# Optimization experiments

Hardware: AMD Instinct MI355X
Metric: run time of the kernel (lower is better)

Reference implementation:

```python
import jax, jax.numpy as jnp
import numpy as np

B, S, D = 16, 1024, 512
H = 2048
E = 16
TOP_K = 4


def setup_inputs() -> dict:
    key = jax.random.key(0)
    ks = jax.random.split(key, 8)
    scale = 0.02
    x = jax.random.normal(ks[0], (B, S, D), dtype=jnp.float32)
    router_w = jax.random.normal(ks[1], (D, E), dtype=jnp.float32) * scale
    router_b = jax.random.normal(ks[2], (E,), dtype=jnp.float32) * scale
    w1 = jax.random.normal(ks[3], (E, D, H), dtype=jnp.float32) * scale
    b1 = jax.random.normal(ks[4], (E, H), dtype=jnp.float32) * scale
    w2 = jax.random.normal(ks[5], (E, H, D), dtype=jnp.float32) * scale
    b2 = jax.random.normal(ks[6], (E, D), dtype=jnp.float32) * scale
    return {"x": x, "router_w": router_w, "router_b": router_b,
            "w1": w1, "b1": b1, "w2": w2, "b2": b2}


def reference(x, router_w, router_b, w1, b1, w2, b2):
    # x: [B, S, D] -> flatten tokens
    x_flat = x.reshape(-1, D)                       # [T, D]
    logits = x_flat @ router_w + router_b           # [T, E]
    top_vals, top_idx = jax.lax.top_k(logits, TOP_K)  # [T, K]
    gates = jax.nn.softmax(top_vals, axis=-1)       # softmax over selected experts only
    # Combined per-expert gate weight per token: sum over k slots routed to e.
    onehot = jax.nn.one_hot(top_idx, E, dtype=x.dtype)  # [T, K, E]
    comb = jnp.einsum('tk,tke->te', gates, onehot)      # [T, E]
    out = jnp.zeros_like(x_flat)
    for e in range(E):  # fixed small expert count
        h = jax.nn.relu(x_flat @ w1[e] + b1[e])     # [T, H]
        y = h @ w2[e] + b2[e]                       # [T, D]
        out = out + comb[:, e:e + 1] * y
    return out.reshape(x.shape)
```

## Files before the change

kernel.cpp:

```cpp
#include <hip/hip_runtime.h>
#include <stdint.h>

#define T_TOK 16384
#define DIM 512
#define HID 2048
#define NE 16
#define TOPK 4
#define BM 256
#define BN 256
#define BKT 64
#define PAIR_CAP 69632
#define MAX_TILES 272
#define NB_CNT 64

typedef short s8v __attribute__((ext_vector_type(8)));
typedef float f4v __attribute__((ext_vector_type(4)));
typedef unsigned int u4v __attribute__((ext_vector_type(4)));

__device__ __forceinline__ unsigned short f2bf(float f) {
  unsigned int u = __builtin_bit_cast(unsigned int, f);
  u = (u + 0x7fffu + ((u >> 16) & 1u)) >> 16;
  return (unsigned short)u;
}
__device__ __forceinline__ float bf2f(unsigned short h) {
  return __builtin_bit_cast(float, (unsigned int)h << 16);
}

__device__ __forceinline__ void gload16(const void* g, void* l) {
  __builtin_amdgcn_global_load_lds(
      (const __attribute__((address_space(1))) unsigned int*)(uintptr_t)g,
      (__attribute__((address_space(3))) unsigned int*)(uintptr_t)l,
      16, 0, 0);
}

__global__ __launch_bounds__(256) void k_transpose_cast(const float* __restrict__ src,
                                                        unsigned short* __restrict__ dst,
                                                        int R, int C) {
  __shared__ float tile[32][33];
  size_t zo = (size_t)blockIdx.z * R * C;
  src += zo; dst += zo;
  int c0 = blockIdx.x * 32, r0 = blockIdx.y * 32;
  int tx = threadIdx.x, ty = threadIdx.y;
#pragma unroll
  for (int i = 0; i < 4; ++i)
    tile[ty + 8 * i][tx] = src[(size_t)(r0 + ty + 8 * i) * C + c0 + tx];
  __syncthreads();
#pragma unroll
  for (int i = 0; i < 4; ++i)
    dst[(size_t)(c0 + ty + 8 * i) * R + r0 + tx] = f2bf(tile[tx][ty + 8 * i]);
}

__global__ __launch_bounds__(256) void k_router(const float* __restrict__ x,
                                                const float* __restrict__ rw,
                                                const float* __restrict__ rb,
                                                int* __restrict__ topki,
                                                float* __restrict__ topkg,
                                                unsigned short* __restrict__ xb) {
  int wv = threadIdx.x >> 6, lane = threadIdx.x & 63;
  int t = blockIdx.x * 4 + wv;
  const float* xr = x + (size_t)t * DIM;
  unsigned short* xbr = xb + (size_t)t * DIM;
  double acc[NE];
#pragma unroll
  for (int e = 0; e < NE; ++e) acc[e] = 0.0;
  for (int it = 0; it < DIM / 64; ++it) {
    float xv = xr[it * 64 + lane];
    xbr[it * 64 + lane] = f2bf(xv);
    const float* r = rw + (size_t)(it * 64 + lane) * NE;
#pragma unroll
    for (int e = 0; e < NE; ++e) acc[e] += (double)xv * (double)r[e];
  }
#pragma unroll
  for (int off = 32; off >= 1; off >>= 1) {
#pragma unroll
    for (int e = 0; e < NE; ++e) acc[e] += __shfl_xor(acc[e], off, 64);
  }
  if (lane == 0) {
    float v[NE];
#pragma unroll
    for (int e = 0; e < NE; ++e) v[e] = (float)acc[e] + rb[e];
    int idx[TOPK]; float val[TOPK];
#pragma unroll
    for (int k = 0; k < TOPK; ++k) {
      float best = -1e30f; int bi = 0;
#pragma unroll
      for (int e = 0; e < NE; ++e)
        if (v[e] > best) { best = v[e]; bi = e; }
      idx[k] = bi; val[k] = best; v[bi] = -1e30f;
    }
    float m = val[0], s = 0.f, g[TOPK];
#pragma unroll
    for (int k = 0; k < TOPK; ++k) { g[k] = __expf(val[k] - m); s += g[k]; }
    float inv = 1.f / s;
#pragma unroll
    for (int k = 0; k < TOPK; ++k) {
      topki[t * TOPK + k] = idx[k];
      topkg[t * TOPK + k] = g[k] * inv;
    }
  }
}

__global__ __launch_bounds__(256) void k_count(const int* __restrict__ topki,
                                               int* __restrict__ meta) {
  __shared__ int lcnt[NE];
  int tid = threadIdx.x;
  if (tid < NE) lcnt[tid] = 0;
  __syncthreads();
  int base = blockIdx.x * 1024 + tid * 4;
#pragma unroll
  for (int j = 0; j < 4; ++j) atomicAdd(&lcnt[topki[base + j]], 1);
  __syncthreads();
  if (tid < NE) meta[1056 + blockIdx.x * NE + tid] = lcnt[tid];
}

__global__ __launch_bounds__(256) void k_plan(int* __restrict__ meta,
                                              int* __restrict__ ptok,
                                              float* __restrict__ pgate) {
  __shared__ int cnt_s[NE], po_s[NE + 1];
  int tid = threadIdx.x;
  if (tid < NE) {
    int s = 0;
    for (int b = 0; b < NB_CNT; ++b) s += meta[1056 + b * NE + tid];
    cnt_s[tid] = s;
  }
  __syncthreads();
  if (tid == 0) {
    int off = 0;
    for (int e = 0; e < NE; ++e) {
      po_s[e] = off;
      meta[1 + e] = off;
      off += ((cnt_s[e] + BM - 1) / BM) * BM;
    }
    po_s[NE] = off;
    meta[1 + NE] = off;
    meta[0] = off / BM;
  }
  __syncthreads();
  if (tid < NE) {
    int run = po_s[tid];
    for (int b = 0; b < NB_CNT; ++b) {
      meta[32 + b * NE + tid] = run;
      run += meta[1056 + b * NE + tid];
    }
  }
  for (int e = 0; e < NE; ++e) {
    int start = po_s[e] + cnt_s[e], end = po_s[e + 1];
    for (int i = start + tid; i < end; i += 256) { ptok[i] = 0; pgate[i] = 0.f; }
  }
}

__global__ __launch_bounds__(256) void k_scatter(const int* __restrict__ topki,
                                                 const float* __restrict__ topkg,
                                                 const int* __restrict__ meta,
                                                 int* __restrict__ ptok,
                                                 float* __restrict__ pgate,
                                                 int* __restrict__ sinv) {
  __shared__ int lcnt[NE];
  int tid = threadIdx.x;
  if (tid < NE) lcnt[tid] = 0;
  __syncthreads();
  int base = blockIdx.x * 1024 + tid * 4;
#pragma unroll
  for (int j = 0; j < 4; ++j) {
    int i = base + j;
    int e = topki[i];
    int r = atomicAdd(&lcnt[e], 1);
    int slot = meta[32 + blockIdx.x * NE + e] + r;
    ptok[slot] = i >> 2;
    pgate[slot] = topkg[i];
    sinv[i] = slot;
  }
}


#define MBAR() asm volatile("s_barrier" ::: "memory")
#define EBAR() asm volatile("s_barrier" ::: "memory")
#define SP1() __builtin_amdgcn_s_setprio(1)
#define SP0() __builtin_amdgcn_s_setprio(0)
#define LGK0() do { asm volatile("s_waitcnt lgkmcnt(0)" ::: "memory"); \
                    __builtin_amdgcn_sched_barrier(0); } while (0)
#define VMC(n) asm volatile("s_waitcnt vmcnt(" #n ")" ::: "memory")
#define NOP ((void)0)

#define STG(rg, kt, c) do {                                                            \
    int _k = (kt) * BKT;                                                               \
    if ((rg) < 2) {                                                                    \
      gload16(aP[rg][0] + _k, (char*)&Al[c][0] + (rg) * 16384 + w * 1024);             \
      gload16(aP[rg][1] + _k, (char*)&Al[c][0] + (rg) * 16384 + 8192 + w * 1024);      \
    } else {                                                                           \
      gload16(bP[(rg) - 2][0] + _k, (char*)&Bl[c][0] + ((rg) - 2) * 16384 + w * 1024); \
      gload16(bP[(rg) - 2][1] + _k, (char*)&Bl[c][0] + ((rg) - 2) * 16384 + 8192 + w * 1024); \
    }                                                                                  \
  } while (0)

#define RDA(c, mq) do {                                                                \
    _Pragma("unroll")                                                                  \
    for (int mt = 0; mt < 4; ++mt) {                                                   \
      af[mt][0] = __builtin_bit_cast(s8v, *(const u4v*)&Al[c][(mq) * 8192 + aoff + mt * 1024 + cs0]); \
      af[mt][1] = __builtin_bit_cast(s8v, *(const u4v*)&Al[c][(mq) * 8192 + aoff + mt * 1024 + cs1]); \
    }                                                                                  \
  } while (0)

#define RDB(c, nq) do {                                                                \
    _Pragma("unroll")                                                                  \
    for (int nt = 0; nt < 2; ++nt) {                                                   \
      bfr[nt][0] = __builtin_bit_cast(s8v, *(const u4v*)&Bl[c][(nq) * 8192 + boff + nt * 1024 + cs0]); \
      bfr[nt][1] = __builtin_bit_cast(s8v, *(const u4v*)&Bl[c][(nq) * 8192 + boff + nt * 1024 + cs1]); \
    }                                                                                  \
  } while (0)

#define MMQ(mq, nq) do {                                                               \
    _Pragma("unroll")                                                                  \
    for (int mt = 0; mt < 4; ++mt) {                                                   \
      _Pragma("unroll")                                                                \
      for (int nt = 0; nt < 2; ++nt) {                                                 \
        acc[(mq) * 4 + mt][(nq) * 2 + nt] = __builtin_amdgcn_mfma_f32_16x16x32_bf16(   \
            af[mt][0], bfr[nt][0], acc[(mq) * 4 + mt][(nq) * 2 + nt], 0, 0, 0);        \
        acc[(mq) * 4 + mt][(nq) * 2 + nt] = __builtin_amdgcn_mfma_f32_16x16x32_bf16(   \
            af[mt][1], bfr[nt][1], acc[(mq) * 4 + mt][(nq) * 2 + nt], 0, 0, 0);        \
      }                                                                                \
    }                                                                                  \
  } while (0)

#define PH(c, mq, nq, doA, STAGE, WAITC) do {  \
    if (doA) RDA(c, mq);                       \
    RDB(c, nq);                                \
    STAGE;                                     \
    MBAR();                                    \
    LGK0();                                    \
    SP1(); MMQ(mq, nq); SP0();                 \
    WAITC;                                     \
    EBAR();                                    \
  } while (0)

__global__ __launch_bounds__(512, 2) void k_pipe(const unsigned short* __restrict__ xb,
                                                 const unsigned short* __restrict__ w1t,
                                                 const float* __restrict__ b1,
                                                 const unsigned short* __restrict__ w2t,
                                                 const float* __restrict__ b2,
                                                 const int* __restrict__ ptok,
                                                 const float* __restrict__ pgate,
                                                 const int* __restrict__ meta,
                                                 unsigned short* __restrict__ hdst,
                                                 const unsigned short* __restrict__ hsrc,
                                                 unsigned short* __restrict__ yslot,
                                                 float* __restrict__ out,
                                                 int c1, int c2, int C) {
  __shared__ __align__(16) unsigned short Al[2][BM * BKT];
  __shared__ __align__(16) unsigned short Bl[2][BN * BKT];
  int tid = threadIdx.x;
  int lane = tid & 63, w = tid >> 6;
  int wm = w >> 2, wn = w & 3;
  int lrow = lane & 15, quad = lane >> 4;
  int r7 = lrow & 7;
  int sub = lane >> 3, lg = (lane & 7) ^ sub;

  bool g2 = blockIdx.x < 2;
  int chunk = g2 ? c2 : c1;
  if (chunk < 0) return;
  int tile = chunk * C + blockIdx.y;
  if (tile >= meta[0]) return;
  int row0 = tile * BM;
  int e = 0;
#pragma unroll
  for (int i = 1; i < NE; ++i)
    if (row0 >= meta[1 + i]) e = i;
  int nblock = g2 ? (int)blockIdx.x * BN : ((int)blockIdx.x - 2) * BN;

  const unsigned short* aP[2][2];
  const unsigned short* bP[2][2];
  int NKT;
  if (!g2) {
    NKT = DIM / BKT;
#pragma unroll
    for (int h = 0; h < 2; ++h)
#pragma unroll
      for (int t = 0; t < 2; ++t) {
        int r = h * 128 + t * 64 + w * 8 + sub;
        aP[h][t] = xb + (size_t)ptok[row0 + r] * DIM + lg * 8;
        bP[h][t] = w1t + ((size_t)e * HID + nblock + r) * DIM + lg * 8;
      }
  } else {
    NKT = HID / BKT;
#pragma unroll
    for (int h = 0; h < 2; ++h)
#pragma unroll
      for (int t = 0; t < 2; ++t) {
        int r = h * 128 + t * 64 + w * 8 + sub;
        aP[h][t] = hsrc + ((size_t)blockIdx.y * BM + r) * HID + lg * 8;
        bP[h][t] = w2t + ((size_t)e * DIM + nblock + r) * HID + lg * 8;
      }
  }

  int aoff = (wm * 64 + lrow) * BKT;
  int boff = (wn * 32 + lrow) * BKT;
  int cs0 = (quad ^ r7) * 8;
  int cs1 = ((4 + quad) ^ r7) * 8;

  f4v acc[8][4] = {};
  s8v af[4][2];
  s8v bfr[2][2];

  STG(0, 0, 0); STG(2, 0, 0); STG(1, 0, 0); STG(3, 0, 0);
  STG(0, 1, 1); STG(2, 1, 1);
  VMC(8);
  EBAR();

  int NI = NKT >> 1;
  for (int i = 0; i < NI - 1; ++i) {
    int bt = 2 * i;
    PH(0, 0, 0, true,  STG(1, bt + 1, 1), VMC(6));
    PH(0, 0, 1, false, STG(3, bt + 1, 1), NOP);
    PH(0, 1, 0, true,  STG(0, bt + 2, 0), NOP);
    PH(0, 1, 1, false, STG(2, bt + 2, 0), VMC(8));
    PH(1, 0, 0, true,  STG(1, bt + 2, 0), VMC(6));
    PH(1, 0, 1, false, STG(3, bt + 2, 0), NOP);
    PH(1, 1, 0, true,  STG(0, bt + 3, 1), NOP);
    PH(1, 1, 1, false, STG(2, bt + 3, 1), VMC(8));
  }
  {
    int bt = NKT - 2;
    PH(0, 0, 0, true,  STG(1, bt + 1, 1), VMC(6));
    PH(0, 0, 1, false, STG(3, bt + 1, 1), NOP);
    PH(0, 1, 0, true,  NOP, NOP);
    PH(0, 1, 1, false, NOP, VMC(4));
    PH(1, 0, 0, true,  NOP, VMC(0));
    PH(1, 0, 1, false, NOP, NOP);
    PH(1, 1, 0, true,  NOP, NOP);
    PH(1, 1, 1, false, NOP, NOP);
  }

  if (!g2) {
    size_t hrow0 = (size_t)blockIdx.y * BM;
#pragma unroll
    for (int nq = 0; nq < 2; ++nq) {
#pragma unroll
      for (int nt = 0; nt < 2; ++nt) {
        int gcol = nblock + nq * 128 + wn * 32 + nt * 16 + lrow;
        float bias = b1[e * HID + gcol];
#pragma unroll
        for (int mq = 0; mq < 2; ++mq) {
#pragma unroll
          for (int mt = 0; mt < 4; ++mt) {
#pragma unroll
            for (int j = 0; j < 4; ++j) {
              int grow = mq * 128 + wm * 64 + mt * 16 + quad * 4 + j;
              float v = acc[mq * 4 + mt][nq * 2 + nt][j] + bias;
              hdst[(hrow0 + grow) * HID + gcol] = f2bf(v > 0.f ? v : 0.f);
            }
          }
        }
      }
    }
  } else {
    float bias[2][2];
#pragma unroll
    for (int nq = 0; nq < 2; ++nq)
#pragma unroll
      for (int nt = 0; nt < 2; ++nt)
        bias[nq][nt] = b2[e * DIM + nblock + nq * 128 + wn * 32 + nt * 16 + lrow];
    if (yslot) {
#pragma unroll
      for (int mq = 0; mq < 2; ++mq) {
#pragma unroll
        for (int mt = 0; mt < 4; ++mt) {
#pragma unroll
          for (int j = 0; j < 4; ++j) {
            int p = row0 + mq * 128 + wm * 64 + mt * 16 + quad * 4 + j;
            float g = pgate[p];
            unsigned short* yr = yslot + (size_t)p * DIM + nblock + wn * 32 + lrow;
#pragma unroll
            for (int nq = 0; nq < 2; ++nq)
#pragma unroll
              for (int nt = 0; nt < 2; ++nt)
                yr[nq * 128 + nt * 16] = f2bf(g * (acc[mq * 4 + mt][nq * 2 + nt][j] + bias[nq][nt]));
          }
        }
      }
    } else {
#pragma unroll
      for (int mq = 0; mq < 2; ++mq) {
#pragma unroll
        for (int mt = 0; mt < 4; ++mt) {
#pragma unroll
          for (int j = 0; j < 4; ++j) {
            int p = row0 + mq * 128 + wm * 64 + mt * 16 + quad * 4 + j;
            float g = pgate[p];
            if (g != 0.f) {
              int tok = ptok[p];
              float* orow = out + (size_t)tok * DIM + nblock + wn * 32 + lrow;
#pragma unroll
              for (int nq = 0; nq < 2; ++nq)
#pragma unroll
                for (int nt = 0; nt < 2; ++nt)
                  atomicAdd(orow + nq * 128 + nt * 16, g * (acc[mq * 4 + mt][nq * 2 + nt][j] + bias[nq][nt]));
            }
          }
        }
      }
    }
  }
}

__global__ __launch_bounds__(256) void k_gather(const unsigned short* __restrict__ yslot,
                                                const int* __restrict__ sinv,
                                                float* __restrict__ out) {
  int id = blockIdx.x * 256 + threadIdx.x;
  int t = id >> 7, d4 = (id & 127) << 2;
  int4 s = *(const int4*)(sinv + t * 4);
  int sl[4] = {s.x, s.y, s.z, s.w};
  float sum0 = 0.f, sum1 = 0.f, sum2 = 0.f, sum3 = 0.f;
#pragma unroll
  for (int k = 0; k < 4; ++k) {
    ushort4 v = *(const ushort4*)(yslot + (size_t)sl[k] * DIM + d4);
    sum0 += bf2f(v.x); sum1 += bf2f(v.y); sum2 += bf2f(v.z); sum3 += bf2f(v.w);
  }
  float4 r; r.x = sum0; r.y = sum1; r.z = sum2; r.w = sum3;
  *(float4*)(out + (size_t)t * DIM + d4) = r;
}

extern "C" void kernel_launch(void* const* d_in, const int* in_sizes, int n_in,
                              void* d_out, int out_size, void* d_ws, size_t ws_size,
                              hipStream_t stream) {
  const float* x  = (const float*)d_in[0];
  const float* rw = (const float*)d_in[1];
  const float* rb = (const float*)d_in[2];
  const float* w1 = (const float*)d_in[3];
  const float* b1 = (const float*)d_in[4];
  const float* w2 = (const float*)d_in[5];
  const float* b2 = (const float*)d_in[6];
  float* out = (float*)d_out;
  char* ws = (char*)d_ws;

  size_t o_xb    = 0;
  size_t o_w1t   = o_xb    + (size_t)T_TOK * DIM * 2;
  size_t o_w2t   = o_w1t   + (size_t)NE * DIM * HID * 2;
  size_t o_topki = o_w2t   + (size_t)NE * DIM * HID * 2;
  size_t o_topkg = o_topki + (size_t)T_TOK * TOPK * 4;
  size_t o_meta  = o_topkg + (size_t)T_TOK * TOPK * 4;
  size_t o_ptok  = o_meta  + 16384;
  size_t o_pgate = o_ptok  + (size_t)PAIR_CAP * 4;
  size_t o_sinv  = o_pgate + (size_t)PAIR_CAP * 4;
  size_t o_yslot = o_sinv  + (size_t)T_TOK * TOPK * 4;
  size_t o_hb    = o_yslot + (size_t)PAIR_CAP * DIM * 2;

  unsigned short* xb   = (unsigned short*)(ws + o_xb);
  unsigned short* w1t  = (unsigned short*)(ws + o_w1t);
  unsigned short* w2t  = (unsigned short*)(ws + o_w2t);
  int*            tki  = (int*)(ws + o_topki);
  float*          tkg  = (float*)(ws + o_topkg);
  int*            meta = (int*)(ws + o_meta);
  int*            ptok = (int*)(ws + o_ptok);
  float*          pgt  = (float*)(ws + o_pgate);
  int*            sinv = (int*)(ws + o_sinv);

  size_t tile_h = (size_t)BM * HID * 2;
  size_t avail = ws_size > o_hb ? ws_size - o_hb : 0;
  long Cd = (long)(avail / (2 * tile_h));
  int use_slot = Cd >= 1;

  k_router<<<T_TOK / 4, 256, 0, stream>>>(x, rw, rb, tki, tkg, xb);
  k_transpose_cast<<<dim3(HID / 32, DIM / 32, NE), dim3(32, 8), 0, stream>>>(w1, w1t, DIM, HID);
  k_transpose_cast<<<dim3(DIM / 32, HID / 32, NE), dim3(32, 8), 0, stream>>>(w2, w2t, HID, DIM);
  k_count<<<NB_CNT, 256, 0, stream>>>(tki, meta);
  k_plan<<<1, 256, 0, stream>>>(meta, ptok, pgt);
  k_scatter<<<NB_CNT, 256, 0, stream>>>(tki, tkg, meta, ptok, pgt, sinv);

  if (use_slot) {
    unsigned short* ysl = (unsigned short*)(ws + o_yslot);
    int C = (int)(Cd > MAX_TILES ? MAX_TILES : Cd);
    int n_chunks = (MAX_TILES + C - 1) / C;
    unsigned short* hb0 = (unsigned short*)(ws + o_hb);
    unsigned short* hb1 = hb0 + (size_t)C * BM * HID;
    for (int i = 0; i <= n_chunks; ++i) {
      unsigned short* dst = (i & 1) ? hb1 : hb0;
      unsigned short* src = (i & 1) ? hb0 : hb1;
      int c1 = (i < n_chunks) ? i : -1;
      int c2 = i - 1;
      k_pipe<<<dim3(10, C), 512, 0, stream>>>(xb, w1t, b1, w2t, b2, ptok, pgt, meta,
                                              dst, src, ysl, out, c1, c2, C);
    }
    k_gather<<<T_TOK * DIM / 4 / 256, 256, 0, stream>>>(ysl, sinv, out);
  } else {
    long Cf = (long)((ws_size - o_yslot) / tile_h);
    int C = (int)(Cf < 1 ? 1 : (Cf > MAX_TILES ? MAX_TILES : Cf));
    int n_chunks = (MAX_TILES + C - 1) / C;
    unsigned short* hb = (unsigned short*)(ws + o_yslot);
    hipMemsetAsync(d_out, 0, (size_t)T_TOK * DIM * 4, stream);
    for (int i = 0; i < n_chunks; ++i) {
      k_pipe<<<dim3(10, C), 512, 0, stream>>>(xb, w1t, b1, w2t, b2, ptok, pgt, meta,
                                              hb, hb, nullptr, out, i, -1, C);
      k_pipe<<<dim3(10, C), 512, 0, stream>>>(xb, w1t, b1, w2t, b2, ptok, pgt, meta,
                                              hb, hb, nullptr, out, -1, i, C);
    }
  }
}
```

Baseline: 747.6 us.

## Use persistent blocks with an atomic work queue and a deeper LDS staging pipeline

Replaces the static 2D grid of GEMM tiles with 256 persistent blocks that pull work items from a global atomic counter. Second-GEMM items are ordered first, and per-launch counters are zeroed in the plan kernel. The K-loop is also restructured: B fragments are now held for both halves, and one more stage is issued before the loop, so loads overlap MFMA work more deeply. This aims to balance the uneven per-expert tile counts and cut tail idle time, at the cost of an atomic and a barrier per item plus extra register pressure.

Measured after the change: 676.3 us. 9.5% less time.

```diff
diff --git a/kernel.cpp b/kernel.cpp
--- a/kernel.cpp
+++ b/kernel.cpp
@@ -12,6 +12,7 @@
 #define PAIR_CAP 69632
 #define MAX_TILES 272
 #define NB_CNT 64
+#define QOFF 2080
 
 typedef short s8v __attribute__((ext_vector_type(8)));
 typedef float f4v __attribute__((ext_vector_type(4)));
@@ -118,6 +119,7 @@
                                               float* __restrict__ pgate) {
   __shared__ int cnt_s[NE], po_s[NE + 1];
   int tid = threadIdx.x;
+  for (int i = tid; i < 1024; i += 256) meta[QOFF + i] = 0;
   if (tid < NE) {
     int s = 0;
     for (int b = 0; b < NB_CNT; ++b) s += meta[1056 + b * NE + tid];
@@ -204,8 +206,8 @@
 #define RDB(c, nq) do {                                                                \
     _Pragma("unroll")                                                                  \
     for (int nt = 0; nt < 2; ++nt) {                                                   \
-      bfr[nt][0] = __builtin_bit_cast(s8v, *(const u4v*)&Bl[c][(nq) * 8192 + boff + nt * 1024 + cs0]); \
-      bfr[nt][1] = __builtin_bit_cast(s8v, *(const u4v*)&Bl[c][(nq) * 8192 + boff + nt * 1024 + cs1]); \
+      bfr[nq][nt][0] = __builtin_bit_cast(s8v, *(const u4v*)&Bl[c][(nq) * 8192 + boff + nt * 1024 + cs0]); \
+      bfr[nq][nt][1] = __builtin_bit_cast(s8v, *(const u4v*)&Bl[c][(nq) * 8192 + boff + nt * 1024 + cs1]); \
     }                                                                                  \
   } while (0)
 
@@ -215,39 +217,32 @@
       _Pragma("unroll")                                                                \
       for (int nt = 0; nt < 2; ++nt) {                                                 \
         acc[(mq) * 4 + mt][(nq) * 2 + nt] = __builtin_amdgcn_mfma_f32_16x16x32_bf16(   \
-            af[mt][0], bfr[nt][0], acc[(mq) * 4 + mt][(nq) * 2 + nt], 0, 0, 0);        \
+            af[mt][0], bfr[nq][nt][0], acc[(mq) * 4 + mt][(nq) * 2 + nt], 0, 0, 0);    \
         acc[(mq) * 4 + mt][(nq) * 2 + nt] = __builtin_amdgcn_mfma_f32_16x16x32_bf16(   \
-            af[mt][1], bfr[nt][1], acc[(mq) * 4 + mt][(nq) * 2 + nt], 0, 0, 0);        \
+            af[mt][1], bfr[nq][nt][1], acc[(mq) * 4 + mt][(nq) * 2 + nt], 0, 0, 0);    \
       }                                                                                \
     }                                                                                  \
   } while (0)
 
-#define PH(c, mq, nq, doA, STAGE, WAITC) do {  \
-    if (doA) RDA(c, mq);                       \
-    RDB(c, nq);                                \
-    STAGE;                                     \
-    MBAR();                                    \
-    LGK0();                                    \
-    SP1(); MMQ(mq, nq); SP0();                 \
-    WAITC;                                     \
-    EBAR();                                    \
-  } while (0)
-
-__global__ __launch_bounds__(512, 2) void k_pipe(const unsigned short* __restrict__ xb,
-                                                 const unsigned short* __restrict__ w1t,
-                                                 const float* __restrict__ b1,
-                                                 const unsigned short* __restrict__ w2t,
-                                                 const float* __restrict__ b2,
-                                                 const int* __restrict__ ptok,
-                                                 const float* __restrict__ pgate,
-                                                 const int* __restrict__ meta,
-                                                 unsigned short* __restrict__ hdst,
-                                                 const unsigned short* __restrict__ hsrc,
-                                                 unsigned short* __restrict__ yslot,
-                                                 float* __restrict__ out,
+#define TAIL(mq, nq) do { MBAR(); LGK0(); SP1(); MMQ(mq, nq); SP0(); } while (0)
+
+__global__ __launch_bounds__(512, 2) void k_pipe(const unsigned short* xb,
+                                                 const unsigned short* w1t,
+                                                 const float* b1,
+                                                 const unsigned short* w2t,
+                                                 const float* b2,
+                                                 const int* ptok,
+                                                 const float* pgate,
+                                                 const int* meta,
+                                                 int* qctr,
+                                                 unsigned short* hdst,
+                                                 const unsigned short* hsrc,
+                                                 unsigned short* yslot,
+                                                 float* out,
                                                  int c1, int c2, int C) {
   __shared__ __align__(16) unsigned short Al[2][BM * BKT];
   __shared__ __align__(16) unsigned short Bl[2][BN * BKT];
+  __shared__ int sh_item;
   int tid = threadIdx.x;
   int lane = tid & 63, w = tid >> 6;
   int wm = w >> 2, wn = w & 3;
@@ -255,145 +250,170 @@
   int r7 = lrow & 7;
   int sub = lane >> 3, lg = (lane & 7) ^ sub;
 
-  bool g2 = blockIdx.x < 2;
-  int chunk = g2 ? c2 : c1;
-  if (chunk < 0) return;
-  int tile = chunk * C + blockIdx.y;
-  if (tile >= meta[0]) return;
-  int row0 = tile * BM;
-  int e = 0;
-#pragma unroll
-  for (int i = 1; i < NE; ++i)
-    if (row0 >= meta[1 + i]) e = i;
-  int nblock = g2 ? (int)blockIdx.x * BN : ((int)blockIdx.x - 2) * BN;
-
-  const unsigned short* aP[2][2];
-  const unsigned short* bP[2][2];
-  int NKT;
-  if (!g2) {
-    NKT = DIM / BKT;
-#pragma unroll
-    for (int h = 0; h < 2; ++h)
-#pragma unroll
-      for (int t = 0; t < 2; ++t) {
-        int r = h * 128 + t * 64 + w * 8 + sub;
-        aP[h][t] = xb + (size_t)ptok[row0 + r] * DIM + lg * 8;
-        bP[h][t] = w1t + ((size_t)e * HID + nblock + r) * DIM + lg * 8;
-      }
-  } else {
-    NKT = HID / BKT;
-#pragma unroll
-    for (int h = 0; h < 2; ++h)
-#pragma unroll
-      for (int t = 0; t < 2; ++t) {
-        int r = h * 128 + t * 64 + w * 8 + sub;
-        aP[h][t] = hsrc + ((size_t)blockIdx.y * BM + r) * HID + lg * 8;
-        bP[h][t] = w2t + ((size_t)e * DIM + nblock + r) * HID + lg * 8;
-      }
-  }
-
   int aoff = (wm * 64 + lrow) * BKT;
   int boff = (wn * 32 + lrow) * BKT;
   int cs0 = (quad ^ r7) * 8;
   int cs1 = ((4 + quad) ^ r7) * 8;
 
-  f4v acc[8][4] = {};
-  s8v af[4][2];
-  s8v bfr[2][2];
-
-  STG(0, 0, 0); STG(2, 0, 0); STG(1, 0, 0); STG(3, 0, 0);
-  STG(0, 1, 1); STG(2, 1, 1);
-  VMC(8);
-  EBAR();
-
-  int NI = NKT >> 1;
-  for (int i = 0; i < NI - 1; ++i) {
-    int bt = 2 * i;
-    PH(0, 0, 0, true,  STG(1, bt + 1, 1), VMC(6));
-    PH(0, 0, 1, false, STG(3, bt + 1, 1), NOP);
-    PH(0, 1, 0, true,  STG(0, bt + 2, 0), NOP);
-    PH(0, 1, 1, false, STG(2, bt + 2, 0), VMC(8));
-    PH(1, 0, 0, true,  STG(1, bt + 2, 0), VMC(6));
-    PH(1, 0, 1, false, STG(3, bt + 2, 0), NOP);
-    PH(1, 1, 0, true,  STG(0, bt + 3, 1), NOP);
-    PH(1, 1, 1, false, STG(2, bt + 3, 1), VMC(8));
-  }
-  {
-    int bt = NKT - 2;
-    PH(0, 0, 0, true,  STG(1, bt + 1, 1), VMC(6));
-    PH(0, 0, 1, false, STG(3, bt + 1, 1), NOP);
-    PH(0, 1, 0, true,  NOP, NOP);
-    PH(0, 1, 1, false, NOP, VMC(4));
-    PH(1, 0, 0, true,  NOP, VMC(0));
-    PH(1, 0, 1, false, NOP, NOP);
-    PH(1, 1, 0, true,  NOP, NOP);
-    PH(1, 1, 1, false, NOP, NOP);
-  }
-
-  if (!g2) {
-    size_t hrow0 = (size_t)blockIdx.y * BM;
-#pragma unroll
-    for (int nq = 0; nq < 2; ++nq) {
-#pragma unroll
-      for (int nt = 0; nt < 2; ++nt) {
-        int gcol = nblock + nq * 128 + wn * 32 + nt * 16 + lrow;
-        float bias = b1[e * HID + gcol];
-#pragma unroll
-        for (int mq = 0; mq < 2; ++mq) {
-#pragma unroll
-          for (int mt = 0; mt < 4; ++mt) {
-#pragma unroll
-            for (int j = 0; j < 4; ++j) {
-              int grow = mq * 128 + wm * 64 + mt * 16 + quad * 4 + j;
-              float v = acc[mq * 4 + mt][nq * 2 + nt][j] + bias;
-              hdst[(hrow0 + grow) * HID + gcol] = f2bf(v > 0.f ? v : 0.f);
+  int T = meta[0];
+  int t2 = 0, t1 = 0;
+  if (c2 >= 0) { t2 = T - c2 * C; t2 = t2 < 0 ? 0 : (t2 > C ? C : t2); }
+  if (c1 >= 0) { t1 = T - c1 * C; t1 = t1 < 0 ? 0 : (t1 > C ? C : t1); }
+  int n2 = 2 * t2, nit = n2 + 8 * t1;
+
+  for (;;) {
+    if (tid == 0) sh_item = atomicAdd(qctr, 1);
+    __syncthreads();
+    int it = sh_item;
+    if (it >= nit) break;
+
+    bool g2 = it < n2;
+    int tloc, nb, tile;
+    if (g2) { tloc = it >> 1; nb = (it & 1) * BN; tile = c2 * C + tloc; }
+    else { int j = it - n2; tloc = j >> 3; nb = (j & 7) * BN; tile = c1 * C + tloc; }
+    int row0 = tile * BM;
+    int e = 0;
+#pragma unroll
+    for (int i2 = 1; i2 < NE; ++i2)
+      if (row0 >= meta[1 + i2]) e = i2;
+
+    const unsigned short* aP[2][2];
+    const unsigned short* bP[2][2];
+    int NKT;
+    if (!g2) {
+      NKT = DIM / BKT;
+#pragma unroll
+      for (int h = 0; h < 2; ++h)
+#pragma unroll
+        for (int t = 0; t < 2; ++t) {
+          int r = h * 128 + t * 64 + w * 8 + sub;
+          aP[h][t] = xb + (size_t)ptok[row0 + r] * DIM + lg * 8;
+          bP[h][t] = w1t + ((size_t)e * HID + nb + r) * DIM + lg * 8;
+        }
+    } else {
+      NKT = HID / BKT;
+#pragma unroll
+      for (int h = 0; h < 2; ++h)
+#pragma unroll
+        for (int t = 0; t < 2; ++t) {
+          int r = h * 128 + t * 64 + w * 8 + sub;
+          aP[h][t] = hsrc + ((size_t)tloc * BM + r) * HID + lg * 8;
+          bP[h][t] = w2t + ((size_t)e * DIM + nb + r) * HID + lg * 8;
+        }
+    }
+
+    f4v acc[8][4] = {};
+    s8v af[4][2];
+    s8v bfr[2][2][2];
+
+    STG(0, 0, 0); STG(2, 0, 0); STG(3, 0, 0); STG(1, 0, 0);
+    STG(0, 1, 1); STG(2, 1, 1); STG(3, 1, 1);
+    VMC(4);
+    EBAR();
+
+    int NI = NKT >> 1;
+    for (int i = 0; i < NI - 1; ++i) {
+      int bt = 2 * i;
+      RDA(0, 0); RDB(0, 0); STG(1, bt + 1, 1);
+      TAIL(0, 0); NOP; EBAR();
+      RDB(0, 1); STG(0, bt + 2, 0);
+      TAIL(0, 1); NOP; EBAR();
+      RDA(0, 1); STG(2, bt + 2, 0);
+      TAIL(1, 0); NOP; EBAR();
+      STG(3, bt + 2, 0);
+      TAIL(1, 1); VMC(6); EBAR();
+      RDA(1, 0); RDB(1, 0); STG(1, bt + 2, 0);
+      TAIL(0, 0); NOP; EBAR();
+      RDB(1, 1); STG(0, bt + 3, 1);
+      TAIL(0, 1); NOP; EBAR();
+      RDA(1, 1); STG(2, bt + 3, 1);
+      TAIL(1, 0); NOP; EBAR();
+      STG(3, bt + 3, 1);
+      TAIL(1, 1); VMC(6); EBAR();
+    }
+    {
+      int bt = NKT - 2;
+      RDA(0, 0); RDB(0, 0); STG(1, bt + 1, 1);
+      TAIL(0, 0); NOP; EBAR();
+      RDB(0, 1);
+      TAIL(0, 1); NOP; EBAR();
+      RDA(0, 1);
+      TAIL(1, 0); NOP; EBAR();
+      TAIL(1, 1); VMC(4); EBAR();
+      RDA(1, 0); RDB(1, 0);
+      TAIL(0, 0); VMC(2); EBAR();
+      RDB(1, 1);
+      TAIL(0, 1); VMC(0); EBAR();
+      RDA(1, 1);
+      TAIL(1, 0); NOP; EBAR();
+      TAIL(1, 1); NOP; EBAR();
+    }
+
+    if (!g2) {
+      size_t hrow0 = (size_t)tloc * BM;
+#pragma unroll
+      for (int nq = 0; nq < 2; ++nq) {
+#pragma unroll
+        for (int nt = 0; nt < 2; ++nt) {
+          int gcol = nb + nq * 128 + wn * 32 + nt * 16 + lrow;
+          float bias = b1[e * HID + gcol];
+#pragma unroll
+          for (int mq = 0; mq < 2; ++mq) {
+#pragma unroll
+            for (int mt = 0; mt < 4; ++mt) {
+#pragma unroll
+              for (int j = 0; j < 4; ++j) {
+                int grow = mq * 128 + wm * 64 + mt * 16 + quad * 4 + j;
+                float v = acc[mq * 4 + mt][nq * 2 + nt][j] + bias;
+                hdst[(hrow0 + grow) * HID + gcol] = f2bf(v > 0.f ? v : 0.f);
+              }
             }
           }
         }
       }
-    }
-  } else {
-    float bias[2][2];
-#pragma unroll
-    for (int nq = 0; nq < 2; ++nq)
-#pragma unroll
-      for (int nt = 0; nt < 2; ++nt)
-        bias[nq][nt] = b2[e * DIM + nblock + nq * 128 + wn * 32 + nt * 16 + lrow];
-    if (yslot) {
-#pragma unroll
-      for (int mq = 0; mq < 2; ++mq) {
-#pragma unroll
-        for (int mt = 0; mt < 4; ++mt) {
-#pragma unroll
-          for (int j = 0; j < 4; ++j) {
-            int p = row0 + mq * 128 + wm * 64 + mt * 16 + quad * 4 + j;
-            float g = pgate[p];
-            unsigned short* yr = yslot + (size_t)p * DIM + nblock + wn * 32 + lrow;
-#pragma unroll
-            for (int nq = 0; nq < 2; ++nq)
-#pragma unroll
-              for (int nt = 0; nt < 2; ++nt)
-                yr[nq * 128 + nt * 16] = f2bf(g * (acc[mq * 4 + mt][nq * 2 + nt][j] + bias[nq][nt]));
+    } else {
+      float bias[2][2];
+#pragma unroll
+      for (int nq = 0; nq < 2; ++nq)
+#pragma unroll
+        for (int nt = 0; nt < 2; ++nt)
+          bias[nq][nt] = b2[e * DIM + nb + nq * 128 + wn * 32 + nt * 16 + lrow];
+      if (yslot) {
+#pragma unroll
+        for (int mq = 0; mq < 2; ++mq) {
+#pragma unroll
+          for (int mt = 0; mt < 4; ++mt) {
+#pragma unroll
+            for (int j = 0; j < 4; ++j) {
+              int p = row0 + mq * 128 + wm * 64 + mt * 16 + quad * 4 + j;
+              float g = pgate[p];
+              unsigned short* yr = yslot + (size_t)p * DIM + nb + wn * 32 + lrow;
+#pragma unroll
+              for (int nq = 0; nq < 2; ++nq)
+#pragma unroll
+                for (int nt = 0; nt < 2; ++nt)
+                  yr[nq * 128 + nt * 16] = f2bf(g * (acc[mq * 4 + mt][nq * 2 + nt][j] + bias[nq][nt]));
+            }
           }
         }
-      }
-    } else {
-#pragma unroll
-      for (int mq = 0; mq < 2; ++mq) {
-#pragma unroll
-        for (int mt = 0; mt < 4; ++mt) {
-#pragma unroll
-          for (int j = 0; j < 4; ++j) {
-            int p = row0 + mq * 128 + wm * 64 + mt * 16 + quad * 4 + j;
-            float g = pgate[p];
-            if (g != 0.f) {
-              int tok = ptok[p];
-              float* orow = out + (size_t)tok * DIM + nblock + wn * 32 + lrow;
-#pragma unroll
-              for (int nq = 0; nq < 2; ++nq)
-#pragma unroll
-                for (int nt = 0; nt < 2; ++nt)
-                  atomicAdd(orow + nq * 128 + nt * 16, g * (acc[mq * 4 + mt][nq * 2 + nt][j] + bias[nq][nt]));
+      } else {
+#pragma unroll
+        for (int mq = 0; mq < 2; ++mq) {
+#pragma unroll
+          for (int mt = 0; mt < 4; ++mt) {
+#pragma unroll
+            for (int j = 0; j < 4; ++j) {
+              int p = row0 + mq * 128 + wm * 64 + mt * 16 + quad * 4 + j;
+              float g = pgate[p];
+              if (g != 0.f) {
+                int tok = ptok[p];
+                float* orow = out + (size_t)tok * DIM + nb + wn * 32 + lrow;
+#pragma unroll
+                for (int nq = 0; nq < 2; ++nq)
+#pragma unroll
+                  for (int nt = 0; nt < 2; ++nt)
+                    atomicAdd(orow + nq * 128 + nt * 16, g * (acc[mq * 4 + mt][nq * 2 + nt][j] + bias[nq][nt]));
+              }
             }
           }
         }
@@ -477,8 +497,8 @@
       unsigned short* src = (i & 1) ? hb0 : hb1;
       int c1 = (i < n_chunks) ? i : -1;
       int c2 = i - 1;
-      k_pipe<<<dim3(10, C), 512, 0, stream>>>(xb, w1t, b1, w2t, b2, ptok, pgt, meta,
-                                              dst, src, ysl, out, c1, c2, C);
+      k_pipe<<<256, 512, 0, stream>>>(xb, w1t, b1, w2t, b2, ptok, pgt, meta,
+                                      meta + QOFF + i, dst, src, ysl, out, c1, c2, C);
     }
     k_gather<<<T_TOK * DIM / 4 / 256, 256, 0, stream>>>(ysl, sinv, out);
   } else {
@@ -488,10 +508,10 @@
     unsigned short* hb = (unsigned short*)(ws + o_yslot);
     hipMemsetAsync(d_out, 0, (size_t)T_TOK * DIM * 4, stream);
     for (int i = 0; i < n_chunks; ++i) {
-      k_pipe<<<dim3(10, C), 512, 0, stream>>>(xb, w1t, b1, w2t, b2, ptok, pgt, meta,
-                                              hb, hb, nullptr, out, i, -1, C);
-      k_pipe<<<dim3(10, C), 512, 0, stream>>>(xb, w1t, b1, w2t, b2, ptok, pgt, meta,
-                                              hb, hb, nullptr, out, -1, i, C);
-    }
-  }
-}
+      k_pipe<<<256, 512, 0, stream>>>(xb, w1t, b1, w2t, b2, ptok, pgt, meta,
+                                      meta + QOFF + 2 * i, hb, hb, nullptr, out, i, -1, C);
+      k_pipe<<<256, 512, 0, stream>>>(xb, w1t, b1, w2t, b2, ptok, pgt, meta,
+                                      meta + QOFF + 2 * i + 1, hb, hb, nullptr, out, -1, i, C);
+    }
+  }
+}
```
